# Kernel optimization log

Hardware: AMD Instinct MI355X
Metric: run time of the kernel (lower is better)

## Reference

```python
import jax, jax.numpy as jnp
import numpy as np

B, T, V, H, NH, NLVL = 64, 2048, 256, 64, 4, 2
HD = H // NH  # 16
EPS = 1e-5


def setup_inputs() -> dict:
    key = jax.random.key(0)
    ks = jax.random.split(key, 16)
    s = 0.05
    return {
        "x": jax.random.randint(ks[0], (B, T), 0, V),
        "emb": jax.random.normal(ks[1], (V, H), dtype=jnp.float32) * s,
        # LSTM params, PyTorch gate order i, f, g, o stacked along dim 0
        "w_ih": jax.random.normal(ks[2], (4 * H, H), dtype=jnp.float32) * s,
        "w_hh": jax.random.normal(ks[3], (4 * H, H), dtype=jnp.float32) * s,
        "b_ih": jax.random.normal(ks[4], (4 * H,), dtype=jnp.float32) * s,
        "b_hh": jax.random.normal(ks[5], (4 * H,), dtype=jnp.float32) * s,
        # two MHA levels, packed qkv in_proj like nn.MultiheadAttention
        "wqkv": jax.random.normal(ks[6], (NLVL, 3 * H, H), dtype=jnp.float32) * s,
        "bqkv": jax.random.normal(ks[7], (NLVL, 3 * H), dtype=jnp.float32) * s,
        "wo": jax.random.normal(ks[8], (NLVL, H, H), dtype=jnp.float32) * s,
        "bo": jax.random.normal(ks[9], (NLVL, H), dtype=jnp.float32) * s,
        "ln_g": jnp.ones((H,), dtype=jnp.float32),
        "ln_b": jnp.zeros((H,), dtype=jnp.float32),
        "fc_w": jax.random.normal(ks[10], (V, H), dtype=jnp.float32) * s,
        "fc_b": jax.random.normal(ks[11], (V,), dtype=jnp.float32) * s,
    }


def _lstm(x, w_ih, w_hh, b_ih, b_hh):
    # x: (B, T, H) -> (B, T, H); single layer, PyTorch gate order i,f,g,o
    b = x.shape[0]
    h0 = jnp.zeros((b, H), x.dtype)
    c0 = jnp.zeros((b, H), x.dtype)

    def step(carry, xt):
        h, c = carry
        g = xt @ w_ih.T + b_ih + h @ w_hh.T + b_hh  # (B, 4H)
        i, f, gg, o = jnp.split(g, 4, axis=-1)
        c = jax.nn.sigmoid(f) * c + jax.nn.sigmoid(i) * jnp.tanh(gg)
        h = jax.nn.sigmoid(o) * jnpp_tanh(c) if False else jax.nn.sigmoid(o) * jnp.tanh(c)
        return (h, c), h

    _, hs = jax.lax.scan(step, (h0, c0), jnp.swapaxes(x, 0, 1))  # (T, B, H)
    return jnp.swapaxes(hs, 0, 1)


def _mha(x, wqkv, bqkv, wo, bo):
    # Faithful to nn.MultiheadAttention with batch_first=False:
    # x: (L, N, E) where here L = batch dim of lstm_out, N = seq dim.
    L, N, E = x.shape
    qkv = x @ wqkv.T + bqkv  # (L, N, 3E)
    q, k, v = jnp.split(qkv, 3, axis=-1)
    q = q.reshape(L, N, NH, HD)
    k = k.reshape(L, N, NH, HD)
    v = v.reshape(L, N, NH, HD)
    scale = jnp.asarray(1.0 / np.sqrt(HD), x.dtype)
    att = jax.nn.softmax(jnp.einsum('lnhd,mnhd->nhlm', q, k) * scale, axis=-1)
    o = jnp.einsum('nhlm,mnhd->lnhd', att, v).reshape(L, N, E)
    return o @ wo.T + bo


def reference(x, emb, w_ih, w_hh, b_ih, b_hh, wqkv, bqkv, wo, bo, ln_g, ln_b, fc_w, fc_b):
    h = emb[x]  # (B, T, H)
    h = _lstm(h, w_ih, w_hh, b_ih, b_hh)  # (B, T, H)
    for l in range(NLVL):
        h = _mha(h, wqkv[l], bqkv[l], wo[l], bo[l])
    mu = jnp.mean(h, axis=-1, keepdims=True)
    var = jnp.mean(jnp.square(h - mu), axis=-1, keepdims=True)  # biased, like torch LN
    hn = (h - mu) * jax.lax.rsqrt(var + EPS) * ln_g + ln_b
    return hn @ fc_w.T + fc_b  # (B, T, V)
```

## Files before the change

kernel.cpp:

```cpp
#include <hip/hip_runtime.h>

enum { TT = 2048, HH = 64, BB = 64, GG = 256, VV = 256 };

static __device__ __forceinline__ void bar_lds(){
  asm volatile("s_waitcnt lgkmcnt(0)\n\ts_barrier" ::: "memory");
}

#define RL(H,k) __int_as_float(__builtin_amdgcn_readlane(__float_as_int(H), (k)))
#define FMA4(acc, W, H, B) do{ \
  acc = fmaf((W).x, RL(H,(B)+0), acc); \
  acc = fmaf((W).y, RL(H,(B)+1), acc); \
  acc = fmaf((W).z, RL(H,(B)+2), acc); \
  acc = fmaf((W).w, RL(H,(B)+3), acc); }while(0)
#define MAC4(acc, U, X) do{ \
  acc = fmaf((U).x, (X).x, acc); \
  acc = fmaf((U).y, (X).y, acc); \
  acc = fmaf((U).z, (X).z, acc); \
  acc = fmaf((U).w, (X).w, acc); }while(0)
#define PINW(W) asm volatile("" : "+v"((W).x), "+v"((W).y), "+v"((W).z), "+v"((W).w))

__global__ __launch_bounds__(256) void k_embw(const float* __restrict__ emb,
                                              const float* __restrict__ w_ih,
                                              const float* __restrict__ b_ih,
                                              const float* __restrict__ b_hh,
                                              float* __restrict__ embW){
  int v = blockIdx.x, g = threadIdx.x;
  __shared__ float e[HH];
  if (g < HH) e[g] = emb[v*HH + g];
  bar_lds();
  float acc = b_ih[g] + b_hh[g];
  const float* wr = w_ih + g*HH;
#pragma unroll
  for (int k = 0; k < HH; k += 4){
    float4 w4 = *(const float4*)(wr + k);
    acc = fmaf(e[k],   w4.x, acc); acc = fmaf(e[k+1], w4.y, acc);
    acc = fmaf(e[k+2], w4.z, acc); acc = fmaf(e[k+3], w4.w, acc);
  }
  embW[v*GG + g] = acc;
}

__global__ __attribute__((amdgpu_waves_per_eu(1, 1)))
__launch_bounds__(256) void k_lstm(const int* __restrict__ x,
                                   const float* __restrict__ embW,
                                   const float* __restrict__ w_hh,
                                   float* __restrict__ hout){
  int b = blockIdx.x, tid = threadIdx.x;
  int q = tid >> 6, l = tid & 63;
  int gate = l >> 4, e = q*16 + (l & 15);
  int row  = gate*64 + e;
  __shared__ __align__(16) float hbuf[2][HH];
  const float4* W4 = (const float4*)(w_hh + row*HH);
  float4 w0  = W4[0],  w1  = W4[1],  w2  = W4[2],  w3  = W4[3];
  float4 w4_ = W4[4],  w5  = W4[5],  w6  = W4[6],  w7  = W4[7];
  float4 w8  = W4[8],  w9  = W4[9],  w10 = W4[10], w11 = W4[11];
  float4 w12 = W4[12], w13 = W4[13], w14 = W4[14], w15 = W4[15];
  PINW(w0);  PINW(w1);  PINW(w2);  PINW(w3);
  PINW(w4_); PINW(w5);  PINW(w6);  PINW(w7);
  PINW(w8);  PINW(w9);  PINW(w10); PINW(w11);
  PINW(w12); PINW(w13); PINW(w14); PINW(w15);
  if (tid < HH) hbuf[0][tid] = 0.f;
  float c = 0.f;
  const int* xb = x + b*TT;
  int i0 = xb[0];
  float gx = embW[i0*GG + row];
  int i1 = xb[1];
  const bool g2 = (gate == 2);
  float* houtb = hout + (size_t)b*TT*HH;
  bar_lds();
  for (int t = 0; t < TT; t++){
    float hv = hbuf[t & 1][l];
    float gxn = embW[i1*GG + row];
    int inx = xb[(t + 2 < TT) ? (t + 2) : (TT - 1)];
    float a0 = gx, a1 = 0.f, a2 = 0.f, a3 = 0.f;
    FMA4(a0, w0,  hv, 0);  FMA4(a0, w1,  hv, 4);  FMA4(a0, w2,  hv, 8);  FMA4(a0, w3,  hv, 12);
    FMA4(a1, w4_, hv, 16); FMA4(a1, w5,  hv, 20); FMA4(a1, w6,  hv, 24); FMA4(a1, w7,  hv, 28);
    FMA4(a2, w8,  hv, 32); FMA4(a2, w9,  hv, 36); FMA4(a2, w10, hv, 40); FMA4(a2, w11, hv, 44);
    FMA4(a3, w12, hv, 48); FMA4(a3, w13, hv, 52); FMA4(a3, w14, hv, 56); FMA4(a3, w15, hv, 60);
    float acc = (a0 + a1) + (a2 + a3);
    float arg = g2 ? (2.f*acc) : acc;
    float s   = 1.f/(1.f + __expf(-arg));
    float val = g2 ? fmaf(2.f, s, -1.f) : s;
    float vi = val;
    float vf = __shfl_xor(val, 16);
    float vg = __shfl_xor(val, 32);
    float vo = __shfl_xor(val, 48);
    c = fmaf(vf, c, vi*vg);
    float th = 1.f - 2.f/(__expf(2.f*c) + 1.f);
    float h  = vo*th;
    if (l < 16){
      hbuf[(t + 1) & 1][e] = h;
      houtb[(size_t)t*HH + e] = h;
    }
    bar_lds();
    gx = gxn; i1 = inx;
  }
}

__global__ __launch_bounds__(256, 1) void k_mha(const float* __restrict__ hin,
                                                const float* __restrict__ wqkv,
                                                const float* __restrict__ bqkv,
                                                const float* __restrict__ wo,
                                                const float* __restrict__ bo,
                                                float* __restrict__ hout){
  int t = blockIdx.x, tid = threadIdx.x;
  __shared__ float xta[BB][HH];
  __shared__ float qkvs[BB][192];

  int tw = (tid < 192) ? tid : 0;
  const float4* wp = (const float4*)(wqkv + tw*HH);
  float4 u0  = wp[0],  u1  = wp[1],  u2  = wp[2],  u3  = wp[3];
  float4 u4  = wp[4],  u5  = wp[5],  u6  = wp[6],  u7  = wp[7];
  float4 u8  = wp[8],  u9  = wp[9],  u10 = wp[10], u11 = wp[11];
  float4 u12 = wp[12], u13 = wp[13], u14 = wp[14], u15 = wp[15];
  PINW(u0);  PINW(u1);  PINW(u2);  PINW(u3);
  PINW(u4);  PINW(u5);  PINW(u6);  PINW(u7);
  PINW(u8);  PINW(u9);  PINW(u10); PINW(u11);
  PINW(u12); PINW(u13); PINW(u14); PINW(u15);
  float bq = bqkv[tw];
  {
    int r = tid >> 2, q = tid & 3;
    const float* p = hin + (size_t)(r*TT + t)*HH + q*16;
#pragma unroll
    for (int j = 0; j < 16; j += 4)
      *(float4*)&xta[r][q*16 + j] = *(const float4*)(p + j);
  }
  bar_lds();
  if (tid < 192){
#pragma unroll 4
    for (int b = 0; b < BB; b++){
      const float4* xp = (const float4*)&xta[b][0];
      float acc = bq;
      float4 xv;
      xv = xp[0];  MAC4(acc, u0,  xv);
      xv = xp[1];  MAC4(acc, u1,  xv);
      xv = xp[2];  MAC4(acc, u2,  xv);
      xv = xp[3];  MAC4(acc, u3,  xv);
      xv = xp[4];  MAC4(acc, u4,  xv);
      xv = xp[5];  MAC4(acc, u5,  xv);
      xv = xp[6];  MAC4(acc, u6,  xv);
      xv = xp[7];  MAC4(acc, u7,  xv);
      xv = xp[8];  MAC4(acc, u8,  xv);
      xv = xp[9];  MAC4(acc, u9,  xv);
      xv = xp[10]; MAC4(acc, u10, xv);
      xv = xp[11]; MAC4(acc, u11, xv);
      xv = xp[12]; MAC4(acc, u12, xv);
      xv = xp[13]; MAC4(acc, u13, xv);
      xv = xp[14]; MAC4(acc, u14, xv);
      xv = xp[15]; MAC4(acc, u15, xv);
      qkvs[b][tid] = acc;
    }
  }
  bar_lds();
  {
    int hd = tid >> 6, l = tid & 63;
    int qo = hd*16, ko = 64 + hd*16, vo = 128 + hd*16;
    float4 q0 = *(const float4*)&qkvs[l][qo];
    float4 q1 = *(const float4*)&qkvs[l][qo+4];
    float4 q2 = *(const float4*)&qkvs[l][qo+8];
    float4 q3 = *(const float4*)&qkvs[l][qo+12];
    float S[BB];
#pragma unroll
    for (int m = 0; m < BB; m++){
      float4 k0 = *(const float4*)&qkvs[m][ko];
      float4 k1 = *(const float4*)&qkvs[m][ko+4];
      float4 k2 = *(const float4*)&qkvs[m][ko+8];
      float4 k3 = *(const float4*)&qkvs[m][ko+12];
      float d;
      d = q0.x*k0.x;         d = fmaf(q0.y,k0.y,d); d = fmaf(q0.z,k0.z,d); d = fmaf(q0.w,k0.w,d);
      d = fmaf(q1.x,k1.x,d); d = fmaf(q1.y,k1.y,d); d = fmaf(q1.z,k1.z,d); d = fmaf(q1.w,k1.w,d);
      d = fmaf(q2.x,k2.x,d); d = fmaf(q2.y,k2.y,d); d = fmaf(q2.z,k2.z,d); d = fmaf(q2.w,k2.w,d);
      d = fmaf(q3.x,k3.x,d); d = fmaf(q3.y,k3.y,d); d = fmaf(q3.z,k3.z,d); d = fmaf(q3.w,k3.w,d);
      S[m] = 0.25f*d;
    }
    float mx = S[0];
#pragma unroll
    for (int m = 1; m < BB; m++) mx = fmaxf(mx, S[m]);
    float sum = 0.f;
#pragma unroll
    for (int m = 0; m < BB; m++){ S[m] = __expf(S[m] - mx); sum += S[m]; }
    float inv = 1.f/sum;
    float4 a0 = make_float4(0,0,0,0), a1 = a0, a2 = a0, a3 = a0;
#pragma unroll
    for (int m = 0; m < BB; m++){
      float s = S[m];
      float4 v0 = *(const float4*)&qkvs[m][vo];
      float4 v1 = *(const float4*)&qkvs[m][vo+4];
      float4 v2 = *(const float4*)&qkvs[m][vo+8];
      float4 v3 = *(const float4*)&qkvs[m][vo+12];
      a0.x = fmaf(s,v0.x,a0.x); a0.y = fmaf(s,v0.y,a0.y); a0.z = fmaf(s,v0.z,a0.z); a0.w = fmaf(s,v0.w,a0.w);
      a1.x = fmaf(s,v1.x,a1.x); a1.y = fmaf(s,v1.y,a1.y); a1.z = fmaf(s,v1.z,a1.z); a1.w = fmaf(s,v1.w,a1.w);
      a2.x = fmaf(s,v2.x,a2.x); a2.y = fmaf(s,v2.y,a2.y); a2.z = fmaf(s,v2.z,a2.z); a2.w = fmaf(s,v2.w,a2.w);
      a3.x = fmaf(s,v3.x,a3.x); a3.y = fmaf(s,v3.y,a3.y); a3.z = fmaf(s,v3.z,a3.z); a3.w = fmaf(s,v3.w,a3.w);
    }
    a0.x*=inv; a0.y*=inv; a0.z*=inv; a0.w*=inv;
    a1.x*=inv; a1.y*=inv; a1.z*=inv; a1.w*=inv;
    a2.x*=inv; a2.y*=inv; a2.z*=inv; a2.w*=inv;
    a3.x*=inv; a3.y*=inv; a3.z*=inv; a3.w*=inv;
    bar_lds();
    *(float4*)&xta[l][qo]    = a0;
    *(float4*)&xta[l][qo+4]  = a1;
    *(float4*)&xta[l][qo+8]  = a2;
    *(float4*)&xta[l][qo+12] = a3;
  }
  bar_lds();
  {
    int c = tid & 63, wg = tid >> 6;
    const float4* wop = (const float4*)(wo + c*HH);
    float4 o0  = wop[0],  o1  = wop[1],  o2  = wop[2],  o3  = wop[3];
    float4 o4  = wop[4],  o5  = wop[5],  o6  = wop[6],  o7  = wop[7];
    float4 o8  = wop[8],  o9  = wop[9],  o10 = wop[10], o11 = wop[11];
    float4 o12 = wop[12], o13 = wop[13], o14 = wop[14], o15 = wop[15];
    PINW(o0);  PINW(o1);  PINW(o2);  PINW(o3);
    PINW(o4);  PINW(o5);  PINW(o6);  PINW(o7);
    PINW(o8);  PINW(o9);  PINW(o10); PINW(o11);
    PINW(o12); PINW(o13); PINW(o14); PINW(o15);
    float bo4 = bo[c];
#pragma unroll 2
    for (int j = 0; j < 16; j++){
      int b = wg*16 + j;
      const float4* xp = (const float4*)&xta[b][0];
      float acc = bo4;
      float4 xv;
      xv = xp[0];  MAC4(acc, o0,  xv);
      xv = xp[1];  MAC4(acc, o1,  xv);
      xv = xp[2];  MAC4(acc, o2,  xv);
      xv = xp[3];  MAC4(acc, o3,  xv);
      xv = xp[4];  MAC4(acc, o4,  xv);
      xv = xp[5];  MAC4(acc, o5,  xv);
      xv = xp[6];  MAC4(acc, o6,  xv);
      xv = xp[7];  MAC4(acc, o7,  xv);
      xv = xp[8];  MAC4(acc, o8,  xv);
      xv = xp[9];  MAC4(acc, o9,  xv);
      xv = xp[10]; MAC4(acc, o10, xv);
      xv = xp[11]; MAC4(acc, o11, xv);
      xv = xp[12]; MAC4(acc, o12, xv);
      xv = xp[13]; MAC4(acc, o13, xv);
      xv = xp[14]; MAC4(acc, o14, xv);
      xv = xp[15]; MAC4(acc, o15, xv);
      hout[(size_t)(b*TT + t)*HH + c] = acc;
    }
  }
}

__global__ __launch_bounds__(256, 1) void k_fc(const float* __restrict__ hin,
                                               const float* __restrict__ ln_g,
                                               const float* __restrict__ ln_b,
                                               const float* __restrict__ fc_w,
                                               const float* __restrict__ fc_b,
                                               float* __restrict__ out){
  int tid = threadIdx.x;
  __shared__ float tile[64][68];
  __shared__ float ps[64][4];
  __shared__ float pq[64][4];
  __shared__ float mu[64], rs[64];
  const float4* fwp = (const float4*)(fc_w + tid*HH);
  const float4* gvp = (const float4*)ln_g;
  const float4* bvp = (const float4*)ln_b;
  float wsum = 0.f, bias2 = fc_b[tid];
  float4 w0, w1, w2, w3, w4_, w5, w6, w7, w8, w9, w10, w11, w12, w13, w14, w15;
#define LNW(Wn, i) do{ \
    float4 fw = fwp[i]; float4 gv = gvp[i]; float4 bv = bvp[i]; \
    bias2 = fmaf(bv.x, fw.x, bias2); bias2 = fmaf(bv.y, fw.y, bias2); \
    bias2 = fmaf(bv.z, fw.z, bias2); bias2 = fmaf(bv.w, fw.w, bias2); \
    Wn = make_float4(gv.x*fw.x, gv.y*fw.y, gv.z*fw.z, gv.w*fw.w); \
    wsum += Wn.x + Wn.y + Wn.z + Wn.w; PINW(Wn); }while(0)
  LNW(w0,0);  LNW(w1,1);  LNW(w2,2);  LNW(w3,3);
  LNW(w4_,4); LNW(w5,5);  LNW(w6,6);  LNW(w7,7);
  LNW(w8,8);  LNW(w9,9);  LNW(w10,10); LNW(w11,11);
  LNW(w12,12); LNW(w13,13); LNW(w14,14); LNW(w15,15);
#undef LNW
  int r = tid >> 2, q = tid & 3;
  for (int ti = 0; ti < 4; ti++){
    int rowbase = blockIdx.x*256 + ti*64;
    const float* p = hin + (size_t)(rowbase + r)*HH + q*16;
    float xv[16];
#pragma unroll
    for (int j = 0; j < 16; j += 4)
      *(float4*)&xv[j] = *(const float4*)(p + j);
    float s1 = 0.f, s2 = 0.f;
#pragma unroll
    for (int j = 0; j < 16; j++){ s1 += xv[j]; s2 = fmaf(xv[j], xv[j], s2); }
#pragma unroll
    for (int j = 0; j < 16; j += 4)
      *(float4*)&tile[r][q*16 + j] = *(const float4*)&xv[j];
    ps[r][q] = s1; pq[r][q] = s2;
    bar_lds();
    if (tid < 64){
      float4 a  = *(const float4*)&ps[tid][0];
      float4 b4 = *(const float4*)&pq[tid][0];
      float m = (a.x + a.y + a.z + a.w) * (1.f/64.f);
      float v = (b4.x + b4.y + b4.z + b4.w) * (1.f/64.f) - m*m;
      mu[tid] = m;
      rs[tid] = rsqrtf(v + 1e-5f);
    }
    bar_lds();
#pragma unroll 2
    for (int rr = 0; rr < 64; rr++){
      const float4* tp = (const float4*)&tile[rr][0];
      float acc = 0.f;
      float4 x4;
      x4 = tp[0];  MAC4(acc, w0,  x4);
      x4 = tp[1];  MAC4(acc, w1,  x4);
      x4 = tp[2];  MAC4(acc, w2,  x4);
      x4 = tp[3];  MAC4(acc, w3,  x4);
      x4 = tp[4];  MAC4(acc, w4_, x4);
      x4 = tp[5];  MAC4(acc, w5,  x4);
      x4 = tp[6];  MAC4(acc, w6,  x4);
      x4 = tp[7];  MAC4(acc, w7,  x4);
      x4 = tp[8];  MAC4(acc, w8,  x4);
      x4 = tp[9];  MAC4(acc, w9,  x4);
      x4 = tp[10]; MAC4(acc, w10, x4);
      x4 = tp[11]; MAC4(acc, w11, x4);
      x4 = tp[12]; MAC4(acc, w12, x4);
      x4 = tp[13]; MAC4(acc, w13, x4);
      x4 = tp[14]; MAC4(acc, w14, x4);
      x4 = tp[15]; MAC4(acc, w15, x4);
      float o = rs[rr]*(acc - mu[rr]*wsum) + bias2;
      out[(size_t)(rowbase + rr)*VV + tid] = o;
    }
    bar_lds();
  }
}

extern "C" void kernel_launch(void* const* d_in, const int* in_sizes, int n_in,
                              void* d_out, int out_size, void* d_ws, size_t ws_size,
                              hipStream_t stream){
  (void)in_sizes; (void)n_in; (void)out_size; (void)ws_size;
  const int*   x    = (const int*)d_in[0];
  const float* emb  = (const float*)d_in[1];
  const float* w_ih = (const float*)d_in[2];
  const float* w_hh = (const float*)d_in[3];
  const float* b_ih = (const float*)d_in[4];
  const float* b_hh = (const float*)d_in[5];
  const float* wqkv = (const float*)d_in[6];
  const float* bqkv = (const float*)d_in[7];
  const float* wo   = (const float*)d_in[8];
  const float* bo   = (const float*)d_in[9];
  const float* ln_g = (const float*)d_in[10];
  const float* ln_b = (const float*)d_in[11];
  const float* fc_w = (const float*)d_in[12];
  const float* fc_b = (const float*)d_in[13];

  char* ws = (char*)d_ws;
  float* embW = (float*)ws;
  float* bufA = (float*)(ws + (1<<20));
  float* bufB = bufA + (size_t)BB*TT*HH;

  k_embw<<<VV,  256, 0, stream>>>(emb, w_ih, b_ih, b_hh, embW);
  k_lstm<<<BB,  256, 0, stream>>>(x, embW, w_hh, bufA);
  k_mha <<<TT,  256, 0, stream>>>(bufA, wqkv,          bqkv,       wo,          bo,      bufB);
  k_mha <<<TT,  256, 0, stream>>>(bufB, wqkv + 192*64, bqkv + 192, wo + 64*64,  bo + 64, bufA);
  k_fc  <<<512, 256, 0, stream>>>(bufA, ln_g, ln_b, fc_w, fc_b, (float*)d_out);
}
```

Measured before the change: 1.706 ms.

## Run LSTM recurrence as one wavefront per batch with all four gates per lane

```diff
diff --git a/kernel.cpp b/kernel.cpp
--- a/kernel.cpp
+++ b/kernel.cpp
@@ -6,12 +6,6 @@
   asm volatile("s_waitcnt lgkmcnt(0)\n\ts_barrier" ::: "memory");
 }
 
-#define RL(H,k) __int_as_float(__builtin_amdgcn_readlane(__float_as_int(H), (k)))
-#define FMA4(acc, W, H, B) do{ \
-  acc = fmaf((W).x, RL(H,(B)+0), acc); \
-  acc = fmaf((W).y, RL(H,(B)+1), acc); \
-  acc = fmaf((W).z, RL(H,(B)+2), acc); \
-  acc = fmaf((W).w, RL(H,(B)+3), acc); }while(0)
 #define MAC4(acc, U, X) do{ \
   acc = fmaf((U).x, (X).x, acc); \
   acc = fmaf((U).y, (X).y, acc); \
@@ -40,59 +34,66 @@
 }
 
 __global__ __attribute__((amdgpu_waves_per_eu(1, 1)))
-__launch_bounds__(256) void k_lstm(const int* __restrict__ x,
-                                   const float* __restrict__ embW,
-                                   const float* __restrict__ w_hh,
-                                   float* __restrict__ hout){
-  int b = blockIdx.x, tid = threadIdx.x;
-  int q = tid >> 6, l = tid & 63;
-  int gate = l >> 4, e = q*16 + (l & 15);
-  int row  = gate*64 + e;
-  __shared__ __align__(16) float hbuf[2][HH];
-  const float4* W4 = (const float4*)(w_hh + row*HH);
-  float4 w0  = W4[0],  w1  = W4[1],  w2  = W4[2],  w3  = W4[3];
-  float4 w4_ = W4[4],  w5  = W4[5],  w6  = W4[6],  w7  = W4[7];
-  float4 w8  = W4[8],  w9  = W4[9],  w10 = W4[10], w11 = W4[11];
-  float4 w12 = W4[12], w13 = W4[13], w14 = W4[14], w15 = W4[15];
-  PINW(w0);  PINW(w1);  PINW(w2);  PINW(w3);
-  PINW(w4_); PINW(w5);  PINW(w6);  PINW(w7);
-  PINW(w8);  PINW(w9);  PINW(w10); PINW(w11);
-  PINW(w12); PINW(w13); PINW(w14); PINW(w15);
-  if (tid < HH) hbuf[0][tid] = 0.f;
+__launch_bounds__(64) void k_lstm(const int* __restrict__ x,
+                                  const float* __restrict__ embW,
+                                  const float* __restrict__ w_hh,
+                                  float* __restrict__ hout){
+  int b = blockIdx.x, l = threadIdx.x;
+  __shared__ __align__(16) float hsh[HH];
+  float4 wi[16], wf[16], wg[16], wo4[16];
+  {
+    const float* ri = w_hh + (l      )*HH;
+    const float* rf = w_hh + (l +  64)*HH;
+    const float* rg = w_hh + (l + 128)*HH;
+    const float* ro = w_hh + (l + 192)*HH;
+#pragma unroll
+    for (int k = 0; k < 16; k++){
+      wi[k]  = *(const float4*)(ri + 4*k); PINW(wi[k]);
+      wf[k]  = *(const float4*)(rf + 4*k); PINW(wf[k]);
+      wg[k]  = *(const float4*)(rg + 4*k); PINW(wg[k]);
+      wo4[k] = *(const float4*)(ro + 4*k); PINW(wo4[k]);
+    }
+  }
+  hsh[l] = 0.f;
   float c = 0.f;
   const int* xb = x + b*TT;
   int i0 = xb[0];
-  float gx = embW[i0*GG + row];
+  float gi = embW[i0*GG +       l];
+  float gf = embW[i0*GG +  64 + l];
+  float gg = embW[i0*GG + 128 + l];
+  float go = embW[i0*GG + 192 + l];
   int i1 = xb[1];
-  const bool g2 = (gate == 2);
   float* houtb = hout + (size_t)b*TT*HH;
-  bar_lds();
+  const float4* hp = (const float4*)hsh;
   for (int t = 0; t < TT; t++){
-    float hv = hbuf[t & 1][l];
-    float gxn = embW[i1*GG + row];
+    float gi_n = embW[i1*GG +       l];
+    float gf_n = embW[i1*GG +  64 + l];
+    float gg_n = embW[i1*GG + 128 + l];
+    float go_n = embW[i1*GG + 192 + l];
     int inx = xb[(t + 2 < TT) ? (t + 2) : (TT - 1)];
-    float a0 = gx, a1 = 0.f, a2 = 0.f, a3 = 0.f;
-    FMA4(a0, w0,  hv, 0);  FMA4(a0, w1,  hv, 4);  FMA4(a0, w2,  hv, 8);  FMA4(a0, w3,  hv, 12);
-    FMA4(a1, w4_, hv, 16); FMA4(a1, w5,  hv, 20); FMA4(a1, w6,  hv, 24); FMA4(a1, w7,  hv, 28);
-    FMA4(a2, w8,  hv, 32); FMA4(a2, w9,  hv, 36); FMA4(a2, w10, hv, 40); FMA4(a2, w11, hv, 44);
-    FMA4(a3, w12, hv, 48); FMA4(a3, w13, hv, 52); FMA4(a3, w14, hv, 56); FMA4(a3, w15, hv, 60);
-    float acc = (a0 + a1) + (a2 + a3);
-    float arg = g2 ? (2.f*acc) : acc;
-    float s   = 1.f/(1.f + __expf(-arg));
-    float val = g2 ? fmaf(2.f, s, -1.f) : s;
-    float vi = val;
-    float vf = __shfl_xor(val, 16);
-    float vg = __shfl_xor(val, 32);
-    float vo = __shfl_xor(val, 48);
+    float ai = gi, af = gf, ag = gg, ao = go;
+#pragma unroll
+    for (int k = 0; k < 16; k++){
+      float4 hv = hp[k];
+      ai = fmaf(wi[k].x,  hv.x, ai); ai = fmaf(wi[k].y,  hv.y, ai);
+      ai = fmaf(wi[k].z,  hv.z, ai); ai = fmaf(wi[k].w,  hv.w, ai);
+      af = fmaf(wf[k].x,  hv.x, af); af = fmaf(wf[k].y,  hv.y, af);
+      af = fmaf(wf[k].z,  hv.z, af); af = fmaf(wf[k].w,  hv.w, af);
+      ag = fmaf(wg[k].x,  hv.x, ag); ag = fmaf(wg[k].y,  hv.y, ag);
+      ag = fmaf(wg[k].z,  hv.z, ag); ag = fmaf(wg[k].w,  hv.w, ag);
+      ao = fmaf(wo4[k].x, hv.x, ao); ao = fmaf(wo4[k].y, hv.y, ao);
+      ao = fmaf(wo4[k].z, hv.z, ao); ao = fmaf(wo4[k].w, hv.w, ao);
+    }
+    float vi = 1.f/(1.f + __expf(-ai));
+    float vf = 1.f/(1.f + __expf(-af));
+    float vg = 1.f - 2.f/(__expf(2.f*ag) + 1.f);
+    float vo = 1.f/(1.f + __expf(-ao));
     c = fmaf(vf, c, vi*vg);
     float th = 1.f - 2.f/(__expf(2.f*c) + 1.f);
     float h  = vo*th;
-    if (l < 16){
-      hbuf[(t + 1) & 1][e] = h;
-      houtb[(size_t)t*HH + e] = h;
-    }
-    bar_lds();
-    gx = gxn; i1 = inx;
+    hsh[l] = h;
+    houtb[(size_t)t*HH + l] = h;
+    gi = gi_n; gf = gf_n; gg = gg_n; go = go_n; i1 = inx;
   }
 }
 
@@ -347,7 +348,7 @@
   float* bufB = bufA + (size_t)BB*TT*HH;
 
   k_embw<<<VV,  256, 0, stream>>>(emb, w_ih, b_ih, b_hh, embW);
-  k_lstm<<<BB,  256, 0, stream>>>(x, embW, w_hh, bufA);
+  k_lstm<<<BB,   64, 0, stream>>>(x, embW, w_hh, bufA);
   k_mha <<<TT,  256, 0, stream>>>(bufA, wqkv,          bqkv,       wo,          bo,      bufB);
   k_mha <<<TT,  256, 0, stream>>>(bufB, wqkv + 192*64, bqkv + 192, wo + 64*64,  bo + 64, bufA);
   k_fc  <<<512, 256, 0, stream>>>(bufA, ln_g, ln_b, fc_w, fc_b, (float*)d_out);
```

Result: slower. 3.136 ms (+83.8%).

## Read LSTM hidden state via LDS float4 and drop LDS staging in MHA/FC

Applied to the files above, without the earlier changes.

```diff
diff --git a/kernel.cpp b/kernel.cpp
--- a/kernel.cpp
+++ b/kernel.cpp
@@ -6,12 +6,6 @@
   asm volatile("s_waitcnt lgkmcnt(0)\n\ts_barrier" ::: "memory");
 }
 
-#define RL(H,k) __int_as_float(__builtin_amdgcn_readlane(__float_as_int(H), (k)))
-#define FMA4(acc, W, H, B) do{ \
-  acc = fmaf((W).x, RL(H,(B)+0), acc); \
-  acc = fmaf((W).y, RL(H,(B)+1), acc); \
-  acc = fmaf((W).z, RL(H,(B)+2), acc); \
-  acc = fmaf((W).w, RL(H,(B)+3), acc); }while(0)
 #define MAC4(acc, U, X) do{ \
   acc = fmaf((U).x, (X).x, acc); \
   acc = fmaf((U).y, (X).y, acc); \
@@ -68,14 +62,27 @@
   float* houtb = hout + (size_t)b*TT*HH;
   bar_lds();
   for (int t = 0; t < TT; t++){
-    float hv = hbuf[t & 1][l];
+    const float4* hp = (const float4*)hbuf[t & 1];
     float gxn = embW[i1*GG + row];
     int inx = xb[(t + 2 < TT) ? (t + 2) : (TT - 1)];
     float a0 = gx, a1 = 0.f, a2 = 0.f, a3 = 0.f;
-    FMA4(a0, w0,  hv, 0);  FMA4(a0, w1,  hv, 4);  FMA4(a0, w2,  hv, 8);  FMA4(a0, w3,  hv, 12);
-    FMA4(a1, w4_, hv, 16); FMA4(a1, w5,  hv, 20); FMA4(a1, w6,  hv, 24); FMA4(a1, w7,  hv, 28);
-    FMA4(a2, w8,  hv, 32); FMA4(a2, w9,  hv, 36); FMA4(a2, w10, hv, 40); FMA4(a2, w11, hv, 44);
-    FMA4(a3, w12, hv, 48); FMA4(a3, w13, hv, 52); FMA4(a3, w14, hv, 56); FMA4(a3, w15, hv, 60);
+    float4 hv;
+    hv = hp[0];  MAC4(a0, w0,  hv);
+    hv = hp[1];  MAC4(a0, w1,  hv);
+    hv = hp[2];  MAC4(a0, w2,  hv);
+    hv = hp[3];  MAC4(a0, w3,  hv);
+    hv = hp[4];  MAC4(a1, w4_, hv);
+    hv = hp[5];  MAC4(a1, w5,  hv);
+    hv = hp[6];  MAC4(a1, w6,  hv);
+    hv = hp[7];  MAC4(a1, w7,  hv);
+    hv = hp[8];  MAC4(a2, w8,  hv);
+    hv = hp[9];  MAC4(a2, w9,  hv);
+    hv = hp[10]; MAC4(a2, w10, hv);
+    hv = hp[11]; MAC4(a2, w11, hv);
+    hv = hp[12]; MAC4(a3, w12, hv);
+    hv = hp[13]; MAC4(a3, w13, hv);
+    hv = hp[14]; MAC4(a3, w14, hv);
+    hv = hp[15]; MAC4(a3, w15, hv);
     float acc = (a0 + a1) + (a2 + a3);
     float arg = g2 ? (2.f*acc) : acc;
     float s   = 1.f/(1.f + __expf(-arg));
@@ -118,17 +125,14 @@
   PINW(u12); PINW(u13); PINW(u14); PINW(u15);
   float bq = bqkv[tw];
   {
-    int r = tid >> 2, q = tid & 3;
-    const float* p = hin + (size_t)(r*TT + t)*HH + q*16;
-#pragma unroll
-    for (int j = 0; j < 16; j += 4)
-      *(float4*)&xta[r][q*16 + j] = *(const float4*)(p + j);
-  }
-  bar_lds();
+    int r = tid >> 2, qq = tid & 3;
+    float4 warm = *(const float4*)(hin + (size_t)(r*TT + t)*HH + qq*16);
+    asm volatile("" :: "v"(warm.x), "v"(warm.y), "v"(warm.z), "v"(warm.w));
+  }
   if (tid < 192){
 #pragma unroll 4
     for (int b = 0; b < BB; b++){
-      const float4* xp = (const float4*)&xta[b][0];
+      const float4* xp = (const float4*)(hin + (size_t)(b*TT + t)*HH);
       float acc = bq;
       float4 xv;
       xv = xp[0];  MAC4(acc, u0,  xv);
@@ -196,7 +200,6 @@
     a1.x*=inv; a1.y*=inv; a1.z*=inv; a1.w*=inv;
     a2.x*=inv; a2.y*=inv; a2.z*=inv; a2.w*=inv;
     a3.x*=inv; a3.y*=inv; a3.z*=inv; a3.w*=inv;
-    bar_lds();
     *(float4*)&xta[l][qo]    = a0;
     *(float4*)&xta[l][qo+4]  = a1;
     *(float4*)&xta[l][qo+8]  = a2;
@@ -249,7 +252,6 @@
                                                const float* __restrict__ fc_b,
                                                float* __restrict__ out){
   int tid = threadIdx.x;
-  __shared__ float tile[64][68];
   __shared__ float ps[64][4];
   __shared__ float pq[64][4];
   __shared__ float mu[64], rs[64];
@@ -280,9 +282,6 @@
     float s1 = 0.f, s2 = 0.f;
 #pragma unroll
     for (int j = 0; j < 16; j++){ s1 += xv[j]; s2 = fmaf(xv[j], xv[j], s2); }
-#pragma unroll
-    for (int j = 0; j < 16; j += 4)
-      *(float4*)&tile[r][q*16 + j] = *(const float4*)&xv[j];
     ps[r][q] = s1; pq[r][q] = s2;
     bar_lds();
     if (tid < 64){
@@ -296,7 +295,7 @@
     bar_lds();
 #pragma unroll 2
     for (int rr = 0; rr < 64; rr++){
-      const float4* tp = (const float4*)&tile[rr][0];
+      const float4* tp = (const float4*)(hin + (size_t)(rowbase + rr)*HH);
       float acc = 0.f;
       float4 x4;
       x4 = tp[0];  MAC4(acc, w0,  x4);
```

Result: slower. 2.141 ms (+25.5%).
